# Optimization experiments

Measured on AMD Instinct MI355X. Metric: run time of the kernel, lower is better.

## Reference

```python
import jax, jax.numpy as jnp
import numpy as np

D_MODEL = 512
D_INNER = 1024   # expand=2
D_STATE = 16
D_CONV = 4
DT_RANK = 32     # ceil(d_model/16)
B, L = 2, 2048


def _params(kbase):
    kk = jax.random.split(kbase, 9)
    n = lambda k, s, sc: jax.random.normal(k, s, jnp.float32) * sc
    return dict(
        Win=n(kk[0], (2 * D_INNER, D_MODEL), D_MODEL ** -0.5),
        convw=n(kk[1], (D_INNER, 1, D_CONV), 0.2),
        convb=n(kk[2], (D_INNER,), 0.02),
        Wx=n(kk[3], (DT_RANK + 2 * D_STATE, D_INNER), D_INNER ** -0.5),
        Wdt=n(kk[4], (D_INNER, DT_RANK), DT_RANK ** -0.5),
        dtb=n(kk[5], (D_INNER,), 0.1),
        Alog=n(kk[6], (D_INNER, D_STATE), 0.5),
        Dp=n(kk[7], (D_INNER,), 1.0),
        Wout=n(kk[8], (D_MODEL, D_INNER), D_INNER ** -0.5),
    )


def setup_inputs() -> dict:
    key = jax.random.key(0)
    k0, kf, kr = jax.random.split(key, 3)
    inp = {"hidden_states": jax.random.normal(k0, (B, L, D_MODEL), jnp.float32)}
    for name, v in _params(kf).items():
        inp[name + "_f"] = v
    for name, v in _params(kr).items():
        inp[name + "_r"] = v
    return inp


def _mamba(x, Win, convw, convb, Wx, Wdt, dtb, Alog, Dp, Wout):
    # x: (B, L, D_MODEL)
    Bb = x.shape[0]
    xz = jnp.einsum('bld,ed->ble', x, Win)            # (B, L, 2*D_INNER)
    xs, z = jnp.split(xz, 2, axis=-1)
    # causal depthwise conv over length
    xc = jnp.swapaxes(xs, 1, 2)                       # (B, D_INNER, L)
    xc = jax.lax.conv_general_dilated(
        xc, convw, (1,), [(D_CONV - 1, 0)], feature_group_count=D_INNER)
    xs = jax.nn.silu(jnp.swapaxes(xc + convb[None, :, None], 1, 2))  # (B, L, D_INNER)
    # input-dependent SSM params
    x_dbl = jnp.einsum('bld,ed->ble', xs, Wx)         # (B, L, DT_RANK+2*D_STATE)
    dt = x_dbl[..., :DT_RANK]
    Bm = x_dbl[..., DT_RANK:DT_RANK + D_STATE]        # (B, L, D_STATE)
    Cm = x_dbl[..., DT_RANK + D_STATE:]               # (B, L, D_STATE)
    dt = jax.nn.softplus(jnp.einsum('blr,dr->bld', dt, Wdt) + dtb)   # (B, L, D_INNER)
    A = -jnp.exp(Alog)                                # (D_INNER, D_STATE), strictly negative
    dA = jnp.exp(dt[..., None] * A)                   # (B, L, D_INNER, D_STATE)
    dBu = dt[..., None] * Bm[:, :, None, :] * xs[..., None]

    def step(h, inp):
        dA_t, dBu_t, C_t = inp
        h = dA_t * h + dBu_t                          # (B, D_INNER, D_STATE)
        return h, jnp.einsum('bds,bs->bd', h, C_t)

    h0 = jnp.zeros((Bb, D_INNER, D_STATE), x.dtype)
    _, ys = jax.lax.scan(
        step, h0,
        (jnp.moveaxis(dA, 1, 0), jnp.moveaxis(dBu, 1, 0), jnp.moveaxis(Cm, 1, 0)))
    y = jnp.moveaxis(ys, 0, 1) + xs * Dp              # (B, L, D_INNER)
    y = y * jax.nn.silu(z)                            # gated output
    return jnp.einsum('bld,ed->ble', y, Wout)         # (B, L, D_MODEL)


def reference(hidden_states,
              Win_f, convw_f, convb_f, Wx_f, Wdt_f, dtb_f, Alog_f, Dp_f, Wout_f,
              Win_r, convw_r, convb_r, Wx_r, Wdt_r, dtb_r, Alog_r, Dp_r, Wout_r):
    out_f = _mamba(hidden_states, Win_f, convw_f, convb_f, Wx_f, Wdt_f, dtb_f,
                   Alog_f, Dp_f, Wout_f)
    out_r = _mamba(hidden_states[:, ::-1, :], Win_r, convw_r, convb_r, Wx_r,
                   Wdt_r, dtb_r, Alog_r, Dp_r, Wout_r)[:, ::-1, :]
    return out_f + out_r  # bidirectional_strategy == 'add'
```

## Files before the change

kernel.cpp:

```cpp
#include <hip/hip_runtime.h>
#include <cmath>

#define B_   2
#define L_   2048
#define DM_  512
#define DI_  1024
#define DS_  16
#define DTR_ 32
#define M_   (B_*L_)
#define NC_  64
#define CL_  32
#define KS_  8
#define LOG2E_ 1.44269504088896340736f
#define LN2_   0.69314718055994530942f

typedef __attribute__((ext_vector_type(8))) short short8;
typedef __attribute__((ext_vector_type(4))) float floatx4;

__device__ inline unsigned short f2bf(float f) {
  unsigned u = __float_as_uint(f);
  unsigned r = (u + 0x7fffu + ((u >> 16) & 1u)) >> 16;
  return (unsigned short)r;
}
__device__ inline float bf2f(unsigned short u) {
  return __uint_as_float(((unsigned)u) << 16);
}
__device__ inline float fexp2(float x) { return __builtin_amdgcn_exp2f(x); }
__device__ inline float flog2(float x) { return __builtin_amdgcn_logf(x); }

__device__ inline void gload_lds16(const unsigned short* g, unsigned short* l) {
  __builtin_amdgcn_global_load_lds(
      (const __attribute__((address_space(1))) void*)g,
      (__attribute__((address_space(3))) void*)l, 16, 0, 0);
}

__global__ __launch_bounds__(256) void gemm1_mfma_k(
    const unsigned short* __restrict__ A,
    const unsigned short* __restrict__ Wf, const unsigned short* __restrict__ Wr,
    unsigned short* __restrict__ Cf, unsigned short* __restrict__ Cr,
    int M, int N, int K)
{
  __shared__ unsigned short At[128 * 32];
  __shared__ unsigned short Wt[128 * 32];
  const unsigned short* W = blockIdx.z ? Wr : Wf;
  unsigned short* C = blockIdx.z ? Cr : Cf;
  const int tid  = threadIdx.x;
  const int w    = tid >> 6;
  const int lane = tid & 63;
  const int wm   = w >> 1, wn = w & 1;
  const int row0 = blockIdx.y * 128, col0 = blockIdx.x * 128;
  const int lrow  = lane >> 2;
  const int lkoff = (lane & 3) * 8;
  const int fr = lane & 15;
  const int fq = (lane >> 4) * 8;

  floatx4 acc[4][4];
#pragma unroll
  for (int i = 0; i < 4; ++i)
#pragma unroll
    for (int j = 0; j < 4; ++j)
#pragma unroll
      for (int r = 0; r < 4; ++r) acc[i][j][r] = 0.f;

  for (int k0 = 0; k0 < K; k0 += 32) {
#pragma unroll
    for (int j = 0; j < 2; ++j) {
      int r = w * 32 + j * 16;
      gload_lds16(A + (size_t)(row0 + r + lrow) * K + k0 + lkoff, At + r * 32);
      gload_lds16(W + (size_t)(col0 + r + lrow) * K + k0 + lkoff, Wt + r * 32);
    }
    __syncthreads();
    short8 af[4], bf[4];
#pragma unroll
    for (int i = 0; i < 4; ++i) {
      af[i] = *(const short8*)&At[(64 * wm + 16 * i + fr) * 32 + fq];
      bf[i] = *(const short8*)&Wt[(64 * wn + 16 * i + fr) * 32 + fq];
    }
#pragma unroll
    for (int i = 0; i < 4; ++i)
#pragma unroll
      for (int j = 0; j < 4; ++j)
        acc[i][j] = __builtin_amdgcn_mfma_f32_16x16x32_bf16(af[i], bf[j], acc[i][j], 0, 0, 0);
    __syncthreads();
  }
#pragma unroll
  for (int i = 0; i < 4; ++i) {
    int rg = row0 + 64 * wm + 16 * i + ((lane >> 4) << 2);
#pragma unroll
    for (int j = 0; j < 4; ++j) {
      int cg = col0 + 64 * wn + 16 * j + (lane & 15);
#pragma unroll
      for (int r = 0; r < 4; ++r)
        C[(size_t)(rg + r) * N + cg] = f2bf(acc[i][j][r]);
    }
  }
}

__global__ __launch_bounds__(256) void gemm4_mfma_k(
    const unsigned short* __restrict__ ybf, const unsigned short* __restrict__ Woutbf,
    const unsigned short* __restrict__ ybr, const unsigned short* __restrict__ Woutbr,
    float* __restrict__ part)
{
  __shared__ unsigned short At[128 * 32];
  __shared__ unsigned short Wt[64 * 32];
  const int tid  = threadIdx.x;
  const int w    = tid >> 6;
  const int lane = tid & 63;
  const int col0 = blockIdx.x * 64;
  const int row0 = blockIdx.y * 128;
  const int z    = blockIdx.z;
  const unsigned short* A = z ? ybr : ybf;
  const unsigned short* W = z ? Woutbr : Woutbf;
  const int lrow  = lane >> 2;
  const int lkoff = (lane & 3) * 8;
  const int fr = lane & 15;
  const int fq = (lane >> 4) * 8;

  floatx4 acc[2][4];
#pragma unroll
  for (int i = 0; i < 2; ++i)
#pragma unroll
    for (int j = 0; j < 4; ++j)
#pragma unroll
      for (int r = 0; r < 4; ++r) acc[i][j][r] = 0.f;

  for (int k0 = 0; k0 < DI_; k0 += 32) {
#pragma unroll
    for (int j = 0; j < 2; ++j) {
      int r = w * 32 + j * 16;
      gload_lds16(A + (size_t)(row0 + r + lrow) * DI_ + k0 + lkoff, At + r * 32);
    }
    {
      int r = w * 16;
      gload_lds16(W + (size_t)(col0 + r + lrow) * DI_ + k0 + lkoff, Wt + r * 32);
    }
    __syncthreads();
    short8 af[2], bf[4];
#pragma unroll
    for (int i = 0; i < 2; ++i)
      af[i] = *(const short8*)&At[(32 * w + 16 * i + fr) * 32 + fq];
#pragma unroll
    for (int j = 0; j < 4; ++j)
      bf[j] = *(const short8*)&Wt[(16 * j + fr) * 32 + fq];
#pragma unroll
    for (int i = 0; i < 2; ++i)
#pragma unroll
      for (int j = 0; j < 4; ++j)
        acc[i][j] = __builtin_amdgcn_mfma_f32_16x16x32_bf16(af[i], bf[j], acc[i][j], 0, 0, 0);
    __syncthreads();
  }
  float* dst = part + (size_t)z * M_ * DM_;
#pragma unroll
  for (int i = 0; i < 2; ++i) {
    int rg = row0 + 32 * w + 16 * i + ((lane >> 4) << 2);
#pragma unroll
    for (int j = 0; j < 4; ++j) {
      int cg = col0 + 16 * j + (lane & 15);
#pragma unroll
      for (int r = 0; r < 4; ++r)
        dst[(size_t)(rg + r) * DM_ + cg] = acc[i][j][r];
    }
  }
}

__global__ __launch_bounds__(256) void add2_k(
    const float* __restrict__ part, float* __restrict__ out)
{
  int g = blockIdx.x * 256 + threadIdx.x;
  float4 a = *(const float4*)(part + (size_t)g * 4);
  float4 b = *(const float4*)(part + (size_t)M_ * DM_ + (size_t)g * 4);
  float4 o = make_float4(a.x + b.x, a.y + b.y, a.z + b.z, a.w + b.w);
  *(float4*)(out + (size_t)g * 4) = o;
}

__global__ __launch_bounds__(256) void gemm2_mfma_k(
    const unsigned short* __restrict__ xsbf, const unsigned short* __restrict__ xsbr,
    const unsigned short* __restrict__ Wxbf, const unsigned short* __restrict__ Wxbr,
    float* __restrict__ part)
{
  __shared__ unsigned short At[128 * 32];
  __shared__ unsigned short Wt[64 * 32];
  const int tid  = threadIdx.x;
  const int w    = tid >> 6;
  const int lane = tid & 63;
  const int ks   = blockIdx.x;
  const int row0 = blockIdx.y * 128;
  const int dir  = blockIdx.z;
  const unsigned short* A = dir ? xsbr : xsbf;
  const unsigned short* W = dir ? Wxbr : Wxbf;
  const int kbase = ks * (DI_ / KS_);
  const int lrow  = lane >> 2;
  const int lkoff = (lane & 3) * 8;
  const int fr = lane & 15;
  const int fq = (lane >> 4) * 8;

  floatx4 acc[2][4];
#pragma unroll
  for (int i = 0; i < 2; ++i)
#pragma unroll
    for (int j = 0; j < 4; ++j)
#pragma unroll
      for (int r = 0; r < 4; ++r) acc[i][j][r] = 0.f;

  for (int k0 = 0; k0 < DI_ / KS_; k0 += 32) {
#pragma unroll
    for (int j = 0; j < 2; ++j) {
      int r = w * 32 + j * 16;
      gload_lds16(A + (size_t)(row0 + r + lrow) * DI_ + kbase + k0 + lkoff, At + r * 32);
    }
    {
      int r = w * 16;
      gload_lds16(W + (size_t)(r + lrow) * DI_ + kbase + k0 + lkoff, Wt + r * 32);
    }
    __syncthreads();
    short8 af[2], bf[4];
#pragma unroll
    for (int i = 0; i < 2; ++i)
      af[i] = *(const short8*)&At[(32 * w + 16 * i + fr) * 32 + fq];
#pragma unroll
    for (int j = 0; j < 4; ++j)
      bf[j] = *(const short8*)&Wt[(16 * j + fr) * 32 + fq];
#pragma unroll
    for (int i = 0; i < 2; ++i)
#pragma unroll
      for (int j = 0; j < 4; ++j)
        acc[i][j] = __builtin_amdgcn_mfma_f32_16x16x32_bf16(af[i], bf[j], acc[i][j], 0, 0, 0);
    __syncthreads();
  }
  float* dst = part + (((size_t)dir * KS_ + ks) * M_) * 64;
#pragma unroll
  for (int i = 0; i < 2; ++i) {
    int rg = row0 + 32 * w + 16 * i + ((lane >> 4) << 2);
#pragma unroll
    for (int j = 0; j < 4; ++j) {
      int cg = 16 * j + (lane & 15);
#pragma unroll
      for (int r = 0; r < 4; ++r)
        dst[(size_t)(rg + r) * 64 + cg] = acc[i][j][r];
    }
  }
}

__global__ __launch_bounds__(256) void reduce_part_k(
    const float* __restrict__ part, float* __restrict__ xdf, float* __restrict__ xdr,
    unsigned short* __restrict__ drbf, unsigned short* __restrict__ drbr)
{
  int g = blockIdx.x * 256 + threadIdx.x;
  int n4  = g & 15;
  int m   = (g >> 4) & (M_ - 1);
  int dir = g >> 16;
  const float* p = part + ((size_t)dir * KS_ * M_ + m) * 64 + n4 * 4;
  float4 s = make_float4(0.f, 0.f, 0.f, 0.f);
#pragma unroll
  for (int ks = 0; ks < KS_; ++ks) {
    float4 v = *(const float4*)(p + (size_t)ks * M_ * 64);
    s.x += v.x; s.y += v.y; s.z += v.z; s.w += v.w;
  }
  float* xd = dir ? xdr : xdf;
  *(float4*)(xd + (size_t)m * 64 + n4 * 4) = s;
  if (n4 < 8) {
    unsigned short* dr = dir ? drbr : drbf;
    ushort4 o;
    o.x = f2bf(s.x); o.y = f2bf(s.y); o.z = f2bf(s.z); o.w = f2bf(s.w);
    *(ushort4*)(dr + (size_t)m * 32 + n4 * 4) = o;
  }
}

struct CastArgs {
  const float* src[9];
  unsigned short* dst[9];
  int start[9];
  int n[9];
};

__global__ __launch_bounds__(256) void cast_multi_k(CastArgs a, int total4)
{
  int g = blockIdx.x * 256 + threadIdx.x;
  if (g >= total4) return;
  int e = g * 4;
#pragma unroll 1
  for (int s = 0; s < 9; ++s) {
    if (e < a.start[s] + a.n[s]) {
      int off = e - a.start[s];
      float4 v = *(const float4*)(a.src[s] + off);
      ushort4 o;
      o.x = f2bf(v.x); o.y = f2bf(v.y); o.z = f2bf(v.z); o.w = f2bf(v.w);
      *(ushort4*)(a.dst[s] + off) = o;
      return;
    }
  }
}

__global__ __launch_bounds__(256) void gemm3_mfma_k(
    const unsigned short* __restrict__ drbf, const unsigned short* __restrict__ drbr,
    const unsigned short* __restrict__ Wdtbf, const unsigned short* __restrict__ Wdtbr,
    const float* __restrict__ b0, const float* __restrict__ b1,
    float* __restrict__ C0, float* __restrict__ C1)
{
  __shared__ unsigned short At[128 * 32];
  __shared__ unsigned short Wt[128 * 32];
  const unsigned short* A = blockIdx.z ? drbr : drbf;
  const unsigned short* W = blockIdx.z ? Wdtbr : Wdtbf;
  const float* bias = blockIdx.z ? b1 : b0;
  float* C = blockIdx.z ? C1 : C0;
  const int tid  = threadIdx.x;
  const int w    = tid >> 6;
  const int lane = tid & 63;
  const int wm   = w >> 1, wn = w & 1;
  const int row0 = blockIdx.y * 128, col0 = blockIdx.x * 128;
  const int lrow  = lane >> 2;
  const int lkoff = (lane & 3) * 8;
  const int fr = lane & 15;
  const int fq = (lane >> 4) * 8;

#pragma unroll
  for (int j = 0; j < 2; ++j) {
    int r = w * 32 + j * 16;
    gload_lds16(A + (size_t)(row0 + r + lrow) * DTR_ + lkoff, At + r * 32);
    gload_lds16(W + (size_t)(col0 + r + lrow) * DTR_ + lkoff, Wt + r * 32);
  }
  __syncthreads();
  short8 af[4], bf[4];
#pragma unroll
  for (int i = 0; i < 4; ++i) {
    af[i] = *(const short8*)&At[(64 * wm + 16 * i + fr) * 32 + fq];
    bf[i] = *(const short8*)&Wt[(64 * wn + 16 * i + fr) * 32 + fq];
  }
  floatx4 acc[4][4];
#pragma unroll
  for (int i = 0; i < 4; ++i)
#pragma unroll
    for (int j = 0; j < 4; ++j) {
#pragma unroll
      for (int r = 0; r < 4; ++r) acc[i][j][r] = 0.f;
      acc[i][j] = __builtin_amdgcn_mfma_f32_16x16x32_bf16(af[i], bf[j], acc[i][j], 0, 0, 0);
    }
#pragma unroll
  for (int i = 0; i < 4; ++i) {
    int rg = row0 + 64 * wm + 16 * i + ((lane >> 4) << 2);
#pragma unroll
    for (int j = 0; j < 4; ++j) {
      int cg = col0 + 64 * wn + 16 * j + (lane & 15);
      float bv = bias[cg];
#pragma unroll
      for (int r = 0; r < 4; ++r) {
        float v = acc[i][j][r] + bv;
        float e = fexp2(-fabsf(v) * LOG2E_);
        float sp = fmaxf(v, 0.f) + LN2_ * flog2(1.f + e);
        C[(size_t)(rg + r) * DI_ + cg] = sp;
      }
    }
  }
}

__global__ __launch_bounds__(256) void conv_silu_k(
    const unsigned short* __restrict__ xzbf, const unsigned short* __restrict__ xzbr,
    const float* __restrict__ cwf, const float* __restrict__ cbf,
    const float* __restrict__ cwr, const float* __restrict__ cbr,
    unsigned short* __restrict__ xsbf, unsigned short* __restrict__ xsbr)
{
  int bid = blockIdx.x;
  int t   = bid & (L_ - 1);
  int b   = (bid >> 11) & (B_ - 1);
  int dir = bid >> 12;
  const unsigned short* xz = dir ? xzbr : xzbf;
  const float* cw = dir ? cwr : cwf;
  const float* cb = dir ? cbr : cbf;
  unsigned short* xsb = dir ? xsbr : xsbf;
  int d0 = threadIdx.x << 2;
  float wv[4][4];
#pragma unroll
  for (int i = 0; i < 4; ++i) {
    float4 w4 = *(const float4*)(cw + (size_t)(d0 + i) * 4);
    wv[i][0] = w4.x; wv[i][1] = w4.y; wv[i][2] = w4.z; wv[i][3] = w4.w;
  }
  float4 cbv = *(const float4*)(cb + d0);
  float acc[4] = {cbv.x, cbv.y, cbv.z, cbv.w};
#pragma unroll
  for (int j = 0; j < 4; ++j) {
    int tt = dir ? (t + 3 - j) : (t - 3 + j);
    if (tt >= 0 && tt < L_) {
      ushort4 v = *(const ushort4*)(xz + ((size_t)b * L_ + tt) * 2048 + d0);
      acc[0] = fmaf(wv[0][j], bf2f(v.x), acc[0]);
      acc[1] = fmaf(wv[1][j], bf2f(v.y), acc[1]);
      acc[2] = fmaf(wv[2][j], bf2f(v.z), acc[2]);
      acc[3] = fmaf(wv[3][j], bf2f(v.w), acc[3]);
    }
  }
  float4 o;
  o.x = acc[0] * __builtin_amdgcn_rcpf(1.f + fexp2(-acc[0] * LOG2E_));
  o.y = acc[1] * __builtin_amdgcn_rcpf(1.f + fexp2(-acc[1] * LOG2E_));
  o.z = acc[2] * __builtin_amdgcn_rcpf(1.f + fexp2(-acc[2] * LOG2E_));
  o.w = acc[3] * __builtin_amdgcn_rcpf(1.f + fexp2(-acc[3] * LOG2E_));
  ushort4 ob;
  ob.x = f2bf(o.x); ob.y = f2bf(o.y); ob.z = f2bf(o.z); ob.w = f2bf(o.w);
  *(ushort4*)(xsb + ((size_t)b * L_ + t) * DI_ + d0) = ob;
}

__global__ __launch_bounds__(256) void scan_passA_k(
    const float* __restrict__ dtf, const float* __restrict__ dtr,
    const unsigned short* __restrict__ xsbf, const unsigned short* __restrict__ xsbr,
    const float* __restrict__ xdf, const float* __restrict__ xdr,
    const float* __restrict__ Alogf, const float* __restrict__ Alogr,
    float* __restrict__ E, float* __restrict__ dts)
{
  __shared__ float bS[CL_][16];
  int bid  = blockIdx.x;
  int dgrp = bid & 3;
  int c    = (bid >> 2) & (NC_ - 1);
  int b    = (bid >> 8) & 1;
  int dir  = bid >> 9;
  int d    = (dgrp << 8) + threadIdx.x;
  const float* dt = dir ? dtr : dtf;
  const unsigned short* xs = dir ? xsbr : xsbf;
  const float* xd = dir ? xdr : xdf;
  const float* Al = dir ? Alogr : Alogf;
  if (threadIdx.x < CL_ * 4) {
    int li = threadIdx.x >> 2;
    int lc = threadIdx.x & 3;
    *(float4*)&bS[li][lc * 4] =
        *(const float4*)(xd + ((size_t)b * L_ + c * CL_ + li) * 64 + 32 + lc * 4);
  }
  float Ai2[16];
#pragma unroll
  for (int s = 0; s < 16; ++s) Ai2[s] = -__expf(Al[(size_t)d * 16 + s]) * LOG2E_;
  float h[16];
#pragma unroll
  for (int s = 0; s < 16; ++s) h[s] = 0.f;
  int t0 = c * CL_ + (dir ? CL_ - 1 : 0);
  const long sdt = (dir ? -1L : 1L) * DI_;
  const float* dtp = dt + ((size_t)b * L_ + t0) * DI_ + d;
  const unsigned short* xsp = xs + ((size_t)b * L_ + t0) * DI_ + d;
  float dtsum = 0.f;
  __syncthreads();
#pragma unroll 2
  for (int i = 0; i < CL_; ++i) {
    int row = dir ? (CL_ - 1 - i) : i;
    float dtv = *dtp;
    float xv  = bf2f(*xsp);
    float Bv[16];
#pragma unroll
    for (int q = 0; q < 4; ++q) {
      float4 bq = *(const float4*)&bS[row][4 * q];
      Bv[4*q] = bq.x; Bv[4*q+1] = bq.y; Bv[4*q+2] = bq.z; Bv[4*q+3] = bq.w;
    }
    float dtx = dtv * xv;
    dtsum += dtv;
#pragma unroll
    for (int s = 0; s < 16; ++s) {
      float dA = fexp2(dtv * Ai2[s]);
      h[s] = fmaf(dA, h[s], dtx * Bv[s]);
    }
    dtp += sdt; xsp += sdt;
  }
  size_t base = ((((size_t)dir * B_ + b) * NC_ + c) * DI_ + d) * 16;
#pragma unroll
  for (int q = 0; q < 4; ++q)
    *(float4*)(E + base + q * 4) = make_float4(h[4*q], h[4*q+1], h[4*q+2], h[4*q+3]);
  dts[(((size_t)dir * B_ + b) * NC_ + c) * DI_ + d] = dtsum;
}

__global__ __launch_bounds__(256) void scan_prefix_k(
    const float* __restrict__ E, const float* __restrict__ dts,
    const float* __restrict__ Alogf, const float* __restrict__ Alogr,
    float* __restrict__ Hin)
{
  int gid = blockIdx.x * 256 + threadIdx.x;
  int s   = gid & 15;
  int d   = (gid >> 4) & (DI_ - 1);
  int b   = (gid >> 14) & 1;
  int dir = gid >> 15;
  const float* Al = dir ? Alogr : Alogf;
  float Ai2 = -__expf(Al[(size_t)d * 16 + s]) * LOG2E_;
  size_t eb  = (((size_t)dir * B_ + b) * NC_) * DI_ * 16 + (size_t)d * 16 + s;
  size_t db2 = (((size_t)dir * B_ + b) * NC_) * DI_ + d;
  float h = 0.f;
  if (!dir) {
    for (int c = 0; c < NC_; ++c) {
      size_t idx = eb + (size_t)c * DI_ * 16;
      Hin[idx] = h;
      float Pv = fexp2(dts[db2 + (size_t)c * DI_] * Ai2);
      h = fmaf(Pv, h, E[idx]);
    }
  } else {
    for (int c = NC_ - 1; c >= 0; --c) {
      size_t idx = eb + (size_t)c * DI_ * 16;
      Hin[idx] = h;
      float Pv = fexp2(dts[db2 + (size_t)c * DI_] * Ai2);
      h = fmaf(Pv, h, E[idx]);
    }
  }
}

__global__ __launch_bounds__(256) void scan_passC_k(
    const float* __restrict__ dtf, const float* __restrict__ dtr,
    const unsigned short* __restrict__ xsbf, const unsigned short* __restrict__ xsbr,
    const float* __restrict__ xdf, const float* __restrict__ xdr,
    const unsigned short* __restrict__ xzbf, const unsigned short* __restrict__ xzbr,
    const float* __restrict__ Alogf, const float* __restrict__ Alogr,
    const float* __restrict__ Dpf, const float* __restrict__ Dpr,
    const float* __restrict__ Hin,
    unsigned short* __restrict__ ybf, unsigned short* __restrict__ ybr)
{
  __shared__ float bcS[CL_][32];
  int bid  = blockIdx.x;
  int dgrp = bid & 3;
  int c    = (bid >> 2) & (NC_ - 1);
  int b    = (bid >> 8) & 1;
  int dir  = bid >> 9;
  int d    = (dgrp << 8) + threadIdx.x;
  const float* dt  = dir ? dtr : dtf;
  const unsigned short* xs = dir ? xsbr : xsbf;
  const float* xd  = dir ? xdr : xdf;
  const unsigned short* xz = dir ? xzbr : xzbf;
  const float* Al  = dir ? Alogr : Alogf;
  unsigned short* yb = dir ? ybr : ybf;
  float Dpv = (dir ? Dpr : Dpf)[d];
  {
    int li = threadIdx.x >> 3;
    int lc = threadIdx.x & 7;
    *(float4*)&bcS[li][lc * 4] =
        *(const float4*)(xd + ((size_t)b * L_ + c * CL_ + li) * 64 + 32 + lc * 4);
  }
  float Ai2[16];
#pragma unroll
  for (int s = 0; s < 16; ++s) Ai2[s] = -__expf(Al[(size_t)d * 16 + s]) * LOG2E_;
  size_t hb = ((((size_t)dir * B_ + b) * NC_ + c) * DI_ + d) * 16;
  float h[16];
#pragma unroll
  for (int q = 0; q < 4; ++q) {
    float4 hv = *(const float4*)(Hin + hb + q * 4);
    h[4*q] = hv.x; h[4*q+1] = hv.y; h[4*q+2] = hv.z; h[4*q+3] = hv.w;
  }
  int t0 = c * CL_ + (dir ? CL_ - 1 : 0);
  const long sdt = (dir ? -1L : 1L) * DI_;
  const long sz_ = (dir ? -1L : 1L) * 2048;
  const float* dtp = dt + ((size_t)b * L_ + t0) * DI_ + d;
  const unsigned short* xsp = xs + ((size_t)b * L_ + t0) * DI_ + d;
  const unsigned short* zp = xz + ((size_t)b * L_ + t0) * 2048 + DI_ + d;
  unsigned short* ybp = yb + ((size_t)b * L_ + t0) * DI_ + d;
  __syncthreads();
#pragma unroll 2
  for (int i = 0; i < CL_; ++i) {
    int row = dir ? (CL_ - 1 - i) : i;
    float dtv = *dtp;
    float xv  = bf2f(*xsp);
    float z   = bf2f(*zp);
    float Bv[16], Cv[16];
#pragma unroll
    for (int q = 0; q < 4; ++q) {
      float4 bq = *(const float4*)&bcS[row][4 * q];
      float4 cq = *(const float4*)&bcS[row][16 + 4 * q];
      Bv[4*q] = bq.x; Bv[4*q+1] = bq.y; Bv[4*q+2] = bq.z; Bv[4*q+3] = bq.w;
      Cv[4*q] = cq.x; Cv[4*q+1] = cq.y; Cv[4*q+2] = cq.z; Cv[4*q+3] = cq.w;
    }
    float dtx = dtv * xv;
    float yacc = 0.f;
#pragma unroll
    for (int s = 0; s < 16; ++s) {
      float dA = fexp2(dtv * Ai2[s]);
      h[s] = fmaf(dA, h[s], dtx * Bv[s]);
      yacc = fmaf(h[s], Cv[s], yacc);
    }
    float yv = fmaf(xv, Dpv, yacc);
    float sz = z * __builtin_amdgcn_rcpf(1.f + fexp2(-z * LOG2E_));
    *ybp = f2bf(yv * sz);
    dtp += sdt; xsp += sdt; zp += sz_; ybp += sdt;
  }
}

extern "C" void kernel_launch(void* const* d_in, const int* in_sizes, int n_in,
                              void* d_out, int out_size, void* d_ws, size_t ws_size,
                              hipStream_t stream)
{
  const float* x       = (const float*)d_in[0];
  const float* Win_f   = (const float*)d_in[1];
  const float* convw_f = (const float*)d_in[2];
  const float* convb_f = (const float*)d_in[3];
  const float* Wx_f    = (const float*)d_in[4];
  const float* Wdt_f   = (const float*)d_in[5];
  const float* dtb_f   = (const float*)d_in[6];
  const float* Alog_f  = (const float*)d_in[7];
  const float* Dp_f    = (const float*)d_in[8];
  const float* Wout_f  = (const float*)d_in[9];
  const float* Win_r   = (const float*)d_in[10];
  const float* convw_r = (const float*)d_in[11];
  const float* convb_r = (const float*)d_in[12];
  const float* Wx_r    = (const float*)d_in[13];
  const float* Wdt_r   = (const float*)d_in[14];
  const float* dtb_r   = (const float*)d_in[15];
  const float* Alog_r  = (const float*)d_in[16];
  const float* Dp_r    = (const float*)d_in[17];
  const float* Wout_r  = (const float*)d_in[18];
  float* out = (float*)d_out;

  float* ws  = (float*)d_ws;
  float* xdf = ws;
  float* xdr = xdf + (size_t)M_ * 64;
  float* dtf = xdr + (size_t)M_ * 64;
  float* dtr = dtf + (size_t)M_ * DI_;
  float* Eb  = dtr + (size_t)M_ * DI_;
  float* Hb  = Eb + (size_t)2 * B_ * NC_ * DI_ * 16;
  float* dtsb = Hb + (size_t)2 * B_ * NC_ * DI_ * 16;
  float* part2 = Eb;
  float* part4 = Eb;
  unsigned short* xzbf    = (unsigned short*)(dtsb + (size_t)2 * B_ * NC_ * DI_);
  unsigned short* xzbr    = xzbf + (size_t)M_ * 2048;
  unsigned short* xb      = xzbr + (size_t)M_ * 2048;
  unsigned short* Winb_f  = xb + (size_t)M_ * DM_;
  unsigned short* Winb_r  = Winb_f + (size_t)2048 * DM_;
  unsigned short* Woutb_f = Winb_r + (size_t)2048 * DM_;
  unsigned short* Woutb_r = Woutb_f + (size_t)DM_ * DI_;
  unsigned short* ybf     = Woutb_r + (size_t)DM_ * DI_;
  unsigned short* ybr     = ybf + (size_t)M_ * DI_;
  unsigned short* xsbf    = ybr + (size_t)M_ * DI_;
  unsigned short* xsbr    = xsbf + (size_t)M_ * DI_;
  unsigned short* Wxb_f   = xsbr + (size_t)M_ * DI_;
  unsigned short* Wxb_r   = Wxb_f + (size_t)64 * DI_;
  unsigned short* Wdtb_f  = Wxb_r + (size_t)64 * DI_;
  unsigned short* Wdtb_r  = Wdtb_f + (size_t)DI_ * DTR_;
  unsigned short* drbf    = Wdtb_r + (size_t)DI_ * DTR_;
  unsigned short* drbr    = drbf + (size_t)M_ * DTR_;

  dim3 blk(256);

  {
    CastArgs ca;
    ca.src[0] = x;      ca.dst[0] = xb;      ca.n[0] = M_ * DM_;
    ca.src[1] = Win_f;  ca.dst[1] = Winb_f;  ca.n[1] = 2048 * DM_;
    ca.src[2] = Win_r;  ca.dst[2] = Winb_r;  ca.n[2] = 2048 * DM_;
    ca.src[3] = Wout_f; ca.dst[3] = Woutb_f; ca.n[3] = DM_ * DI_;
    ca.src[4] = Wout_r; ca.dst[4] = Woutb_r; ca.n[4] = DM_ * DI_;
    ca.src[5] = Wx_f;   ca.dst[5] = Wxb_f;   ca.n[5] = 64 * DI_;
    ca.src[6] = Wx_r;   ca.dst[6] = Wxb_r;   ca.n[6] = 64 * DI_;
    ca.src[7] = Wdt_f;  ca.dst[7] = Wdtb_f;  ca.n[7] = DI_ * DTR_;
    ca.src[8] = Wdt_r;  ca.dst[8] = Wdtb_r;  ca.n[8] = DI_ * DTR_;
    int st = 0;
    for (int s = 0; s < 9; ++s) { ca.start[s] = st; st += ca.n[s]; }
    int total4 = st / 4;
    cast_multi_k<<<(total4 + 255) / 256, blk, 0, stream>>>(ca, total4);
  }

  gemm1_mfma_k<<<dim3(2048 / 128, M_ / 128, 2), blk, 0, stream>>>(
      xb, Winb_f, Winb_r, xzbf, xzbr, M_, 2048, DM_);

  conv_silu_k<<<2 * B_ * L_, blk, 0, stream>>>(xzbf, xzbr, convw_f, convb_f,
      convw_r, convb_r, xsbf, xsbr);

  gemm2_mfma_k<<<dim3(KS_, M_ / 128, 2), blk, 0, stream>>>(
      xsbf, xsbr, Wxb_f, Wxb_r, part2);
  reduce_part_k<<<(2 * M_ * 16) / 256, blk, 0, stream>>>(part2, xdf, xdr,
      drbf, drbr);

  gemm3_mfma_k<<<dim3(DI_ / 128, M_ / 128, 2), blk, 0, stream>>>(
      drbf, drbr, Wdtb_f, Wdtb_r, dtb_f, dtb_r, dtf, dtr);

  scan_passA_k<<<2 * B_ * NC_ * 4, blk, 0, stream>>>(dtf, dtr, xsbf, xsbr,
      xdf, xdr, Alog_f, Alog_r, Eb, dtsb);
  scan_prefix_k<<<(2 * B_ * DI_ * 16) / 256, blk, 0, stream>>>(
      Eb, dtsb, Alog_f, Alog_r, Hb);
  scan_passC_k<<<2 * B_ * NC_ * 4, blk, 0, stream>>>(dtf, dtr, xsbf, xsbr,
      xdf, xdr, xzbf, xzbr, Alog_f, Alog_r, Dp_f, Dp_r, Hb, ybf, ybr);

  gemm4_mfma_k<<<dim3(DM_ / 64, M_ / 128, 2), blk, 0, stream>>>(
      ybf, Woutb_f, ybr, Woutb_r, part4);
  add2_k<<<(M_ * DM_ / 4) / 256, blk, 0, stream>>>(part4, out);
}
```

Before: 278.5 us.

## Fuse bidirectional output GEMMs with final add and store dt in fp16

The final output projection now accumulates both the forward and reverse directions in one kernel, iterating over both sources into a single accumulator. This removes the fp32 partial buffer and the separate add kernel. The block tile shrinks to 64x64 with a K step of 64. Separately, the softplus dt output is stored as fp16 instead of fp32, which halves dt traffic in both scan passes in exchange for some precision loss.

```diff
diff --git a/kernel.cpp b/kernel.cpp
--- a/kernel.cpp
+++ b/kernel.cpp
@@ -24,6 +24,14 @@
 }
 __device__ inline float bf2f(unsigned short u) {
   return __uint_as_float(((unsigned)u) << 16);
+}
+__device__ inline unsigned short f2h(float f) {
+  _Float16 h = (_Float16)f;
+  return *(unsigned short*)&h;
+}
+__device__ inline float h2f(unsigned short u) {
+  _Float16 h = *(_Float16*)&u;
+  return (float)h;
 }
 __device__ inline float fexp2(float x) { return __builtin_amdgcn_exp2f(x); }
 __device__ inline float flog2(float x) { return __builtin_amdgcn_logf(x); }
@@ -96,81 +104,66 @@
   }
 }
 
-__global__ __launch_bounds__(256) void gemm4_mfma_k(
+__global__ __launch_bounds__(256) void gemm4_fused_k(
     const unsigned short* __restrict__ ybf, const unsigned short* __restrict__ Woutbf,
     const unsigned short* __restrict__ ybr, const unsigned short* __restrict__ Woutbr,
-    float* __restrict__ part)
-{
-  __shared__ unsigned short At[128 * 32];
-  __shared__ unsigned short Wt[64 * 32];
+    float* __restrict__ out)
+{
+  __shared__ unsigned short At[2][64 * 32];
+  __shared__ unsigned short Wt[2][64 * 32];
   const int tid  = threadIdx.x;
   const int w    = tid >> 6;
   const int lane = tid & 63;
   const int col0 = blockIdx.x * 64;
-  const int row0 = blockIdx.y * 128;
-  const int z    = blockIdx.z;
-  const unsigned short* A = z ? ybr : ybf;
-  const unsigned short* W = z ? Woutbr : Woutbf;
+  const int row0 = blockIdx.y * 64;
   const int lrow  = lane >> 2;
   const int lkoff = (lane & 3) * 8;
   const int fr = lane & 15;
   const int fq = (lane >> 4) * 8;
 
-  floatx4 acc[2][4];
-#pragma unroll
-  for (int i = 0; i < 2; ++i)
-#pragma unroll
-    for (int j = 0; j < 4; ++j)
-#pragma unroll
-      for (int r = 0; r < 4; ++r) acc[i][j][r] = 0.f;
-
-  for (int k0 = 0; k0 < DI_; k0 += 32) {
-#pragma unroll
-    for (int j = 0; j < 2; ++j) {
-      int r = w * 32 + j * 16;
-      gload_lds16(A + (size_t)(row0 + r + lrow) * DI_ + k0 + lkoff, At + r * 32);
-    }
-    {
-      int r = w * 16;
-      gload_lds16(W + (size_t)(col0 + r + lrow) * DI_ + k0 + lkoff, Wt + r * 32);
-    }
-    __syncthreads();
-    short8 af[2], bf[4];
-#pragma unroll
-    for (int i = 0; i < 2; ++i)
-      af[i] = *(const short8*)&At[(32 * w + 16 * i + fr) * 32 + fq];
-#pragma unroll
-    for (int j = 0; j < 4; ++j)
-      bf[j] = *(const short8*)&Wt[(16 * j + fr) * 32 + fq];
-#pragma unroll
-    for (int i = 0; i < 2; ++i)
-#pragma unroll
-      for (int j = 0; j < 4; ++j)
-        acc[i][j] = __builtin_amdgcn_mfma_f32_16x16x32_bf16(af[i], bf[j], acc[i][j], 0, 0, 0);
-    __syncthreads();
-  }
-  float* dst = part + (size_t)z * M_ * DM_;
-#pragma unroll
-  for (int i = 0; i < 2; ++i) {
-    int rg = row0 + 32 * w + 16 * i + ((lane >> 4) << 2);
-#pragma unroll
-    for (int j = 0; j < 4; ++j) {
-      int cg = col0 + 16 * j + (lane & 15);
-#pragma unroll
-      for (int r = 0; r < 4; ++r)
-        dst[(size_t)(rg + r) * DM_ + cg] = acc[i][j][r];
-    }
-  }
-}
-
-__global__ __launch_bounds__(256) void add2_k(
-    const float* __restrict__ part, float* __restrict__ out)
-{
-  int g = blockIdx.x * 256 + threadIdx.x;
-  float4 a = *(const float4*)(part + (size_t)g * 4);
-  float4 b = *(const float4*)(part + (size_t)M_ * DM_ + (size_t)g * 4);
-  float4 o = make_float4(a.x + b.x, a.y + b.y, a.z + b.z, a.w + b.w);
-  *(float4*)(out + (size_t)g * 4) = o;
+  floatx4 acc[4];
+#pragma unroll
+  for (int j = 0; j < 4; ++j)
+#pragma unroll
+    for (int r = 0; r < 4; ++r) acc[j][r] = 0.f;
+
+#pragma unroll 1
+  for (int src = 0; src < 2; ++src) {
+    const unsigned short* A = src ? ybr : ybf;
+    const unsigned short* W = src ? Woutbr : Woutbf;
+    for (int k0 = 0; k0 < DI_; k0 += 64) {
+#pragma unroll
+      for (int h = 0; h < 2; ++h) {
+        gload_lds16(A + (size_t)(row0 + 16 * w + lrow) * DI_ + k0 + 32 * h + lkoff,
+                    At[h] + (16 * w) * 32);
+        gload_lds16(W + (size_t)(col0 + 16 * w + lrow) * DI_ + k0 + 32 * h + lkoff,
+                    Wt[h] + (16 * w) * 32);
+      }
+      __syncthreads();
+      short8 af[2], bf[2][4];
+#pragma unroll
+      for (int h = 0; h < 2; ++h) {
+        af[h] = *(const short8*)&At[h][(16 * w + fr) * 32 + fq];
+#pragma unroll
+        for (int j = 0; j < 4; ++j)
+          bf[h][j] = *(const short8*)&Wt[h][(16 * j + fr) * 32 + fq];
+      }
+#pragma unroll
+      for (int h = 0; h < 2; ++h)
+#pragma unroll
+        for (int j = 0; j < 4; ++j)
+          acc[j] = __builtin_amdgcn_mfma_f32_16x16x32_bf16(af[h], bf[h][j], acc[j], 0, 0, 0);
+      __syncthreads();
+    }
+  }
+  const int rg = row0 + 16 * w + ((lane >> 4) << 2);
+#pragma unroll
+  for (int j = 0; j < 4; ++j) {
+    int cg = col0 + 16 * j + (lane & 15);
+#pragma unroll
+    for (int r = 0; r < 4; ++r)
+      out[(size_t)(rg + r) * DM_ + cg] = acc[j][r];
+  }
 }
 
 __global__ __launch_bounds__(256) void gemm2_mfma_k(
@@ -295,14 +288,14 @@
     const unsigned short* __restrict__ drbf, const unsigned short* __restrict__ drbr,
     const unsigned short* __restrict__ Wdtbf, const unsigned short* __restrict__ Wdtbr,
     const float* __restrict__ b0, const float* __restrict__ b1,
-    float* __restrict__ C0, float* __restrict__ C1)
+    unsigned short* __restrict__ C0, unsigned short* __restrict__ C1)
 {
   __shared__ unsigned short At[128 * 32];
   __shared__ unsigned short Wt[128 * 32];
   const unsigned short* A = blockIdx.z ? drbr : drbf;
   const unsigned short* W = blockIdx.z ? Wdtbr : Wdtbf;
   const float* bias = blockIdx.z ? b1 : b0;
-  float* C = blockIdx.z ? C1 : C0;
+  unsigned short* C = blockIdx.z ? C1 : C0;
   const int tid  = threadIdx.x;
   const int w    = tid >> 6;
   const int lane = tid & 63;
@@ -347,7 +340,7 @@
         float v = acc[i][j][r] + bv;
         float e = fexp2(-fabsf(v) * LOG2E_);
         float sp = fmaxf(v, 0.f) + LN2_ * flog2(1.f + e);
-        C[(size_t)(rg + r) * DI_ + cg] = sp;
+        C[(size_t)(rg + r) * DI_ + cg] = f2h(sp);
       }
     }
   }
@@ -398,7 +391,7 @@
 }
 
 __global__ __launch_bounds__(256) void scan_passA_k(
-    const float* __restrict__ dtf, const float* __restrict__ dtr,
+    const unsigned short* __restrict__ dtf, const unsigned short* __restrict__ dtr,
     const unsigned short* __restrict__ xsbf, const unsigned short* __restrict__ xsbr,
     const float* __restrict__ xdf, const float* __restrict__ xdr,
     const float* __restrict__ Alogf, const float* __restrict__ Alogr,
@@ -411,7 +404,7 @@
   int b    = (bid >> 8) & 1;
   int dir  = bid >> 9;
   int d    = (dgrp << 8) + threadIdx.x;
-  const float* dt = dir ? dtr : dtf;
+  const unsigned short* dt = dir ? dtr : dtf;
   const unsigned short* xs = dir ? xsbr : xsbf;
   const float* xd = dir ? xdr : xdf;
   const float* Al = dir ? Alogr : Alogf;
@@ -429,14 +422,14 @@
   for (int s = 0; s < 16; ++s) h[s] = 0.f;
   int t0 = c * CL_ + (dir ? CL_ - 1 : 0);
   const long sdt = (dir ? -1L : 1L) * DI_;
-  const float* dtp = dt + ((size_t)b * L_ + t0) * DI_ + d;
+  const unsigned short* dtp = dt + ((size_t)b * L_ + t0) * DI_ + d;
   const unsigned short* xsp = xs + ((size_t)b * L_ + t0) * DI_ + d;
   float dtsum = 0.f;
   __syncthreads();
 #pragma unroll 2
   for (int i = 0; i < CL_; ++i) {
     int row = dir ? (CL_ - 1 - i) : i;
-    float dtv = *dtp;
+    float dtv = h2f(*dtp);
     float xv  = bf2f(*xsp);
     float Bv[16];
 #pragma unroll
@@ -493,7 +486,7 @@
 }
 
 __global__ __launch_bounds__(256) void scan_passC_k(
-    const float* __restrict__ dtf, const float* __restrict__ dtr,
+    const unsigned short* __restrict__ dtf, const unsigned short* __restrict__ dtr,
     const unsigned short* __restrict__ xsbf, const unsigned short* __restrict__ xsbr,
     const float* __restrict__ xdf, const float* __restrict__ xdr,
     const unsigned short* __restrict__ xzbf, const unsigned short* __restrict__ xzbr,
@@ -509,7 +502,7 @@
   int b    = (bid >> 8) & 1;
   int dir  = bid >> 9;
   int d    = (dgrp << 8) + threadIdx.x;
-  const float* dt  = dir ? dtr : dtf;
+  const unsigned short* dt  = dir ? dtr : dtf;
   const unsigned short* xs = dir ? xsbr : xsbf;
   const float* xd  = dir ? xdr : xdf;
   const unsigned short* xz = dir ? xzbr : xzbf;
@@ -535,7 +528,7 @@
   int t0 = c * CL_ + (dir ? CL_ - 1 : 0);
   const long sdt = (dir ? -1L : 1L) * DI_;
   const long sz_ = (dir ? -1L : 1L) * 2048;
-  const float* dtp = dt + ((size_t)b * L_ + t0) * DI_ + d;
+  const unsigned short* dtp = dt + ((size_t)b * L_ + t0) * DI_ + d;
   const unsigned short* xsp = xs + ((size_t)b * L_ + t0) * DI_ + d;
   const unsigned short* zp = xz + ((size_t)b * L_ + t0) * 2048 + DI_ + d;
   unsigned short* ybp = yb + ((size_t)b * L_ + t0) * DI_ + d;
@@ -543,7 +536,7 @@
 #pragma unroll 2
   for (int i = 0; i < CL_; ++i) {
     int row = dir ? (CL_ - 1 - i) : i;
-    float dtv = *dtp;
+    float dtv = h2f(*dtp);
     float xv  = bf2f(*xsp);
     float z   = bf2f(*zp);
     float Bv[16], Cv[16];
@@ -597,13 +590,12 @@
   float* ws  = (float*)d_ws;
   float* xdf = ws;
   float* xdr = xdf + (size_t)M_ * 64;
-  float* dtf = xdr + (size_t)M_ * 64;
-  float* dtr = dtf + (size_t)M_ * DI_;
-  float* Eb  = dtr + (size_t)M_ * DI_;
+  unsigned short* dtf = (unsigned short*)(xdr + (size_t)M_ * 64);
+  unsigned short* dtr = dtf + (size_t)M_ * DI_;
+  float* Eb  = (float*)(dtr + (size_t)M_ * DI_);
   float* Hb  = Eb + (size_t)2 * B_ * NC_ * DI_ * 16;
   float* dtsb = Hb + (size_t)2 * B_ * NC_ * DI_ * 16;
   float* part2 = Eb;
-  float* part4 = Eb;
   unsigned short* xzbf    = (unsigned short*)(dtsb + (size_t)2 * B_ * NC_ * DI_);
   unsigned short* xzbr    = xzbf + (size_t)M_ * 2048;
   unsigned short* xb      = xzbr + (size_t)M_ * 2048;
@@ -662,7 +654,6 @@
   scan_passC_k<<<2 * B_ * NC_ * 4, blk, 0, stream>>>(dtf, dtr, xsbf, xsbr,
       xdf, xdr, xzbf, xzbr, Alog_f, Alog_r, Dp_f, Dp_r, Hb, ybf, ybr);
 
-  gemm4_mfma_k<<<dim3(DM_ / 64, M_ / 128, 2), blk, 0, stream>>>(
-      ybf, Woutb_f, ybr, Woutb_r, part4);
-  add2_k<<<(M_ * DM_ / 4) / 256, blk, 0, stream>>>(part4, out);
-}
+  gemm4_fused_k<<<dim3(DM_ / 64, M_ / 64), blk, 0, stream>>>(
+      ybf, Woutb_f, ybr, Woutb_r, out);
+}
```

Result: faster. 270.5 us (-2.9%).
